# Optimization experiments

Measured on AMD Instinct MI355X. Metric: run time of the kernel, lower is better.

## Reference

```python
import jax, jax.numpy as jnp
import numpy as np

HIDDEN = 1024
NUM_HEADS = 16
HOP_NUM = 1023  # seq_len = hop_num + 1 = 1024
ATT_SIZE = HIDDEN // NUM_HEADS
SCALE = ATT_SIZE ** (-0.5)
B, S = 8, HOP_NUM + 1


def setup_inputs() -> dict:
    key = jax.random.key(0)
    ks = jax.random.split(key, 13)
    lim = 1.0 / np.sqrt(HIDDEN)
    return {
        "q": jax.random.normal(ks[0], (B, S, HIDDEN), jnp.float32),
        "k": jax.random.normal(ks[1], (B, S, HIDDEN), jnp.float32),
        "v": jax.random.normal(ks[2], (B, S, HIDDEN), jnp.float32),
        "attn_bias": jax.random.normal(ks[3], (B, 1, S, S), jnp.float32),
        "Wq": jax.random.uniform(ks[4], (HIDDEN, HIDDEN), jnp.float32, -lim, lim),
        "bq": jax.random.uniform(ks[5], (HIDDEN,), jnp.float32, -lim, lim),
        "Wk": jax.random.uniform(ks[6], (HIDDEN, HIDDEN), jnp.float32, -lim, lim),
        "bk": jax.random.uniform(ks[7], (HIDDEN,), jnp.float32, -lim, lim),
        "Wv": jax.random.uniform(ks[8], (HIDDEN, HIDDEN), jnp.float32, -lim, lim),
        "bv": jax.random.uniform(ks[9], (HIDDEN,), jnp.float32, -lim, lim),
        "Wo": jax.random.uniform(ks[10], (HIDDEN, HIDDEN), jnp.float32, -lim, lim),
        "bo": jax.random.uniform(ks[11], (HIDDEN,), jnp.float32, -lim, lim),
        "zoom_bias": jax.random.normal(ks[12], (2 * HOP_NUM + 1, 1), jnp.float32),
    }


def reference(q, k, v, attn_bias, Wq, bq, Wk, bk, Wv, bv, Wo, bo, zoom_bias):
    b, s, _ = q.shape
    # projections -> [b, s, h, d]
    qh = (q @ Wq.T + bq).reshape(b, s, NUM_HEADS, ATT_SIZE)
    kh = (k @ Wk.T + bk).reshape(b, s, NUM_HEADS, ATT_SIZE)
    vh = (v @ Wv.T + bv).reshape(b, s, NUM_HEADS, ATT_SIZE)
    # relative zoom encoding: ze[i, j] = zoom_bias[i - j + hop_num]
    idx = jnp.arange(s)[:, None] - jnp.arange(s)[None, :] + HOP_NUM
    ze = zoom_bias[idx, 0]  # [s, s]
    # scaled dot-product attention with additive zoom bias
    scores = jnp.einsum("bshd,bthd->bhst", qh * SCALE, kh) + ze + attn_bias
    probs = jax.nn.softmax(scores, axis=-1)
    out = jnp.einsum("bhst,bthd->bshd", probs, vh).reshape(b, s, NUM_HEADS * ATT_SIZE)
    return out @ Wo.T + bo
```

## Files before the change

### kernel.cpp

```cpp
#include <hip/hip_runtime.h>
#include <cstdint>


#define SQ   1024
#define HID  1024
#define SCALE 0.125f

typedef __attribute__((ext_vector_type(8))) __bf16 bf16x8;
typedef __attribute__((ext_vector_type(8))) unsigned short ushort8;
typedef __attribute__((ext_vector_type(4))) float  floatx4;

__device__ __forceinline__ float b2f(unsigned short x) {
    return __builtin_bit_cast(float, (uint32_t)x << 16);
}
__device__ __forceinline__ unsigned short f2bf(float f) {
    uint32_t u = __builtin_bit_cast(uint32_t, f);
    u += 0x7fffu + ((u >> 16) & 1u);
    return (unsigned short)(u >> 16);
}

__device__ __forceinline__ void glds16(const void* g, void* l) {
    __builtin_amdgcn_global_load_lds(
        (const __attribute__((address_space(1))) void*)g,
        (__attribute__((address_space(3))) void*)l, 16, 0, 0);
}

__global__ void cvt(const float* __restrict__ s, unsigned short* __restrict__ d,
                    int n4, float scale) {
    const int i = blockIdx.x * blockDim.x + threadIdx.x;
    if (i >= n4) return;
    const floatx4 v = *(const floatx4*)(s + 4 * (size_t)i);
    uint32_t lo = (uint32_t)f2bf(v[0] * scale) | ((uint32_t)f2bf(v[1] * scale) << 16);
    uint32_t hi = (uint32_t)f2bf(v[2] * scale) | ((uint32_t)f2bf(v[3] * scale) << 16);
    ((uint2*)d)[i] = make_uint2(lo, hi);
}

template <bool TRANS>
__global__ __launch_bounds__(256) void gemm_bt(
    const short* __restrict__ A, const short* __restrict__ Bw,
    const float* __restrict__ bias, void* __restrict__ C, size_t cOff, int outF32)
{
    __shared__ __align__(16) short As[4096];
    __shared__ __align__(16) short Bs[4096];

    const int tid = threadIdx.x;
    const int w = tid >> 6, lane = tid & 63;
    const int quad = lane >> 4, c = lane & 15;
    const int wr = w >> 1, wc = w & 1;

    const int nwg = gridDim.x * gridDim.y;
    const int id  = blockIdx.y * gridDim.x + blockIdx.x;
    const int nid = (id & 7) * (nwg >> 3) + (id >> 3);
    const int bn = nid & 7, bm = nid >> 3;

    const short* ag0 = A  + (size_t)(bm * 128 + w * 16 + c) * HID + quad * 8;
    const short* ag1 = ag0 + (size_t)64 * HID;
    const short* bg0 = Bw + (size_t)(bn * 128 + w * 16 + c) * HID + quad * 8;
    const short* bg1 = bg0 + (size_t)64 * HID;

    floatx4 acc[4][4] = {};

    for (int kt = 0; kt < 32; ++kt) {
        __syncthreads();
        glds16(ag0, As + w * 512);
        glds16(ag1, As + (w + 4) * 512);
        glds16(bg0, Bs + w * 512);
        glds16(bg1, Bs + (w + 4) * 512);
        asm volatile("s_waitcnt vmcnt(0)" ::: "memory");
        __syncthreads();
        ag0 += 32; ag1 += 32; bg0 += 32; bg1 += 32;

        bf16x8 a[4], b[4];
#pragma unroll
        for (int i = 0; i < 4; ++i)
            a[i] = *(const bf16x8*)(As + (wr * 4 + i) * 512 + lane * 8);
#pragma unroll
        for (int j = 0; j < 4; ++j)
            b[j] = *(const bf16x8*)(Bs + (wc * 4 + j) * 512 + lane * 8);
#pragma unroll
        for (int i = 0; i < 4; ++i)
#pragma unroll
            for (int j = 0; j < 4; ++j)
                acc[i][j] = __builtin_amdgcn_mfma_f32_16x16x32_bf16(a[i], b[j], acc[i][j], 0, 0, 0);
    }

    float bsv[4];
#pragma unroll
    for (int j = 0; j < 4; ++j)
        bsv[j] = bias[bn * 128 + wc * 64 + j * 16 + c];

#pragma unroll
    for (int i = 0; i < 4; ++i) {
#pragma unroll
        for (int j = 0; j < 4; ++j) {
            const int n = bn * 128 + wc * 64 + j * 16 + c;
#pragma unroll
            for (int r = 0; r < 4; ++r) {
                const int row = bm * 128 + wr * 64 + i * 16 + quad * 4 + r;
                const float val = acc[i][j][r] + bsv[j];
                size_t idx;
                if (TRANS) idx = ((size_t)(row >> 10) * HID + n) * SQ + (row & 1023);
                else       idx = (size_t)row * HID + n;
                if (outF32) ((float*)C)[cOff + idx] = val;
                else        ((unsigned short*)C)[cOff + idx] = f2bf(val);
            }
        }
    }
}

__global__ __launch_bounds__(256) void attn(
    const short* __restrict__ qh, const short* __restrict__ kh,
    const short* __restrict__ vht, const unsigned short* __restrict__ abc,
    const float* __restrict__ zbf, short* __restrict__ aout, int b0)
{
    __shared__ __align__(16) short Kf[4096];
    __shared__ __align__(16) short Vf[4096];
    __shared__ __align__(16) short Ps[4][2304];
    __shared__ float Zs[1152];

    const int tid = threadIdx.x;
    const int w = tid >> 6, lane = tid & 63;
    const int quad = lane >> 4, c = lane & 15;
    const int qb = blockIdx.x, h = blockIdx.y, bl = blockIdx.z;
    const int b = b0 + bl;

    for (int j = tid; j < 1151; j += 256)
        Zs[j] = zbf[qb * 128 + j];

    const size_t blS = (size_t)bl * SQ;

    bf16x8 qa[2][2];
#pragma unroll
    for (int m = 0; m < 2; ++m)
#pragma unroll
        for (int half = 0; half < 2; ++half)
            qa[m][half] = *(const bf16x8*)(qh + (blS + qb * 128 + w * 32 + m * 16 + c) * HID
                                               + h * 64 + half * 32 + quad * 8);

    const short* kg = kh  + (blS + 2 * c + (w & 1)) * HID + h * 64 + (w >> 1) * 32 + quad * 8;
    const short* vg = vht + ((size_t)bl * HID + h * 64 + w * 16 + c) * SQ + quad * 8;
    const size_t bge = ((size_t)b * SQ + qb * 128 + w * 32 + quad * 4) * SQ;

    bf16x8 kv0 = *(const bf16x8*)kg, kv1 = *(const bf16x8*)(kg + 32 * HID);
    bf16x8 vv0 = *(const bf16x8*)vg, vv1 = *(const bf16x8*)(vg + 32);

    floatx4 o[2][4] = {};
    float sume[2][4] = {};

    for (int kt = 0; kt < 16; ++kt) {
        __syncthreads();
        *(bf16x8*)(Kf + w * 512 + lane * 8)       = kv0;
        *(bf16x8*)(Kf + (w + 4) * 512 + lane * 8) = kv1;
        *(bf16x8*)(Vf + w * 512 + lane * 8)       = vv0;
        *(bf16x8*)(Vf + (w + 4) * 512 + lane * 8) = vv1;
        __syncthreads();

        if (kt < 15) {
            kg += 64 * HID; vg += 64;
            kv0 = *(const bf16x8*)kg; kv1 = *(const bf16x8*)(kg + 32 * HID);
            vv0 = *(const bf16x8*)vg; vv1 = *(const bf16x8*)(vg + 32);
        }

        floatx4 sc[2][2][2] = {};
#pragma unroll
        for (int sub = 0; sub < 2; ++sub) {
            bf16x8 kf[2][2];
#pragma unroll
            for (int half = 0; half < 2; ++half)
#pragma unroll
                for (int kb = 0; kb < 2; ++kb)
                    kf[half][kb] = *(const bf16x8*)(Kf + (sub * 4 + half * 2 + kb) * 512 + lane * 8);
#pragma unroll
            for (int m = 0; m < 2; ++m)
#pragma unroll
                for (int kb = 0; kb < 2; ++kb) {
                    sc[m][sub][kb] = __builtin_amdgcn_mfma_f32_16x16x32_bf16(qa[m][0], kf[0][kb], sc[m][sub][kb], 0, 0, 0);
                    sc[m][sub][kb] = __builtin_amdgcn_mfma_f32_16x16x32_bf16(qa[m][1], kf[1][kb], sc[m][sub][kb], 0, 0, 0);
                }
        }

        const int k0 = kt * 64;
#pragma unroll
        for (int m = 0; m < 2; ++m) {
#pragma unroll
            for (int r = 0; r < 4; ++r) {
                const int lrq = w * 32 + m * 16 + quad * 4 + r;
                const int tb = lrq + 1023 - k0;
                const size_t brow = bge + (size_t)(m * 16 + r) * SQ + k0;
#pragma unroll
                for (int sub = 0; sub < 2; ++sub) {
                    const int kl = sub * 32 + 2 * c;
                    const uint32_t bp = *(const uint32_t*)(abc + brow + kl);
                    const float z0 = Zs[tb - kl], z1 = Zs[tb - kl - 1];
                    const float s0 = sc[m][sub][0][r] * SCALE + z0 + b2f((unsigned short)(bp & 0xffffu));
                    const float s1 = sc[m][sub][1][r] * SCALE + z1
                                   + __builtin_bit_cast(float, bp & 0xffff0000u);
                    const float e0 = __expf(s0), e1 = __expf(s1);
                    sume[m][r] += e0 + e1;
                    const uint32_t pp = (uint32_t)f2bf(e0) | ((uint32_t)f2bf(e1) << 16);
                    *(uint32_t*)(&Ps[w][0] + (m * 16 + quad * 4 + r) * 72 + kl) = pp;
                }
            }
        }

#pragma unroll
        for (int sub = 0; sub < 2; ++sub) {
            bf16x8 ap[2];
#pragma unroll
            for (int m = 0; m < 2; ++m)
                ap[m] = *(const bf16x8*)(&Ps[w][0] + (m * 16 + c) * 72 + sub * 32 + quad * 8);
#pragma unroll
            for (int dt = 0; dt < 4; ++dt) {
                const bf16x8 vf = *(const bf16x8*)(Vf + (sub * 4 + dt) * 512 + lane * 8);
#pragma unroll
                for (int m = 0; m < 2; ++m)
                    o[m][dt] = __builtin_amdgcn_mfma_f32_16x16x32_bf16(ap[m], vf, o[m][dt], 0, 0, 0);
            }
        }
    }

#pragma unroll
    for (int m = 0; m < 2; ++m)
#pragma unroll
        for (int r = 0; r < 4; ++r) {
            float s = sume[m][r];
            s += __shfl_xor(s, 1);
            s += __shfl_xor(s, 2);
            s += __shfl_xor(s, 4);
            s += __shfl_xor(s, 8);
            sume[m][r] = 1.0f / s;
        }

#pragma unroll
    for (int m = 0; m < 2; ++m)
#pragma unroll
        for (int dt = 0; dt < 4; ++dt)
#pragma unroll
            for (int r = 0; r < 4; ++r) {
                const size_t row = blS + qb * 128 + w * 32 + m * 16 + quad * 4 + r;
                ((unsigned short*)aout)[row * HID + h * 64 + dt * 16 + c] =
                    f2bf(o[m][dt][r] * sume[m][r]);
            }
}

extern "C" void kernel_launch(void* const* d_in, const int* in_sizes, int n_in,
                              void* d_out, int out_size, void* d_ws, size_t ws_size,
                              hipStream_t stream) {
    const float* q  = (const float*)d_in[0];
    const float* k  = (const float*)d_in[1];
    const float* v  = (const float*)d_in[2];
    const float* ab = (const float*)d_in[3];
    const float* Wq = (const float*)d_in[4];  const float* bq = (const float*)d_in[5];
    const float* Wk = (const float*)d_in[6];  const float* bk = (const float*)d_in[7];
    const float* Wv = (const float*)d_in[8];  const float* bv = (const float*)d_in[9];
    const float* Wo = (const float*)d_in[10]; const float* bo = (const float*)d_in[11];
    const float* zb = (const float*)d_in[12];

    const size_t perB = (size_t)SQ * HID;
    const size_t WN   = (size_t)HID * HID;

    int G = 8;
    while (G > 1 && 24ull * 1024 * 1024 + 8ull * G * perB > ws_size) G >>= 1;

    unsigned short* Wqc = (unsigned short*)d_ws;
    unsigned short* Wkc = Wqc + WN;
    unsigned short* Wvc = Wkc + WN;
    unsigned short* Woc = Wvc + WN;
    unsigned short* abc = Woc + WN;
    short* cb  = (short*)(abc + 8 * perB);
    short* qh  = cb  + (size_t)G * perB;
    short* khp = qh  + (size_t)G * perB;
    short* vht = khp + (size_t)G * perB;
    short* ao  = cb;

    const dim3 bt(256);
    const dim3 gg(8, G * 8);
    const int ngroups = 8 / G;
    const int cn4 = (int)(G * perB / 4);
    const int cgrid = (cn4 + 255) / 256;

    cvt<<<(WN / 4 + 255) / 256, 256, 0, stream>>>(Wq, Wqc, WN / 4, 1.0f);
    cvt<<<(WN / 4 + 255) / 256, 256, 0, stream>>>(Wk, Wkc, WN / 4, 1.0f);
    cvt<<<(WN / 4 + 255) / 256, 256, 0, stream>>>(Wv, Wvc, WN / 4, 1.0f);
    cvt<<<(WN / 4 + 255) / 256, 256, 0, stream>>>(Wo, Woc, WN / 4, 1.0f);
    cvt<<<(8 * perB / 4 + 255) / 256, 256, 0, stream>>>(ab, abc, 8 * perB / 4, 1.0f);

    for (int g = 0; g < ngroups; ++g) {
        const size_t off = (size_t)g * G * perB;
        cvt<<<cgrid, 256, 0, stream>>>(q + off, (unsigned short*)cb, cn4, 1.0f);
        gemm_bt<false><<<gg, bt, 0, stream>>>(cb, (short*)Wqc, bq, qh, 0, 0);
        cvt<<<cgrid, 256, 0, stream>>>(k + off, (unsigned short*)cb, cn4, 1.0f);
        gemm_bt<false><<<gg, bt, 0, stream>>>(cb, (short*)Wkc, bk, khp, 0, 0);
        cvt<<<cgrid, 256, 0, stream>>>(v + off, (unsigned short*)cb, cn4, 1.0f);
        gemm_bt<true ><<<gg, bt, 0, stream>>>(cb, (short*)Wvc, bv, vht, 0, 0);
        attn<<<dim3(8, 16, G), bt, 0, stream>>>(qh, khp, vht, abc, zb, ao, g * G);
        gemm_bt<false><<<gg, bt, 0, stream>>>(ao, (short*)Woc, bo, d_out, off, 1);
    }
}
```

Before: 518.1 us.

## Batch QKV conversion and projection launches, prefetch bias, use exp2 softmax

Merges the three per-projection conversion kernels and the three projection GEMMs into single launches indexed by blockIdx.z, and gives the output GEMM its own f32-only kernel. In attention, the attn_bias tile for the next key block is prefetched into registers one iteration early. The softmax folds log2(e) into the score scale, zoom bias and pre-converted attn_bias so it can use exp2 directly. Extra workspace is needed for three separate converted input buffers, which may shrink the group size on small workspaces, and the register prefetch raises register pressure.

```diff
diff --git a/kernel.cpp b/kernel.cpp
--- a/kernel.cpp
+++ b/kernel.cpp
@@ -4,7 +4,8 @@
 
 #define SQ   1024
 #define HID  1024
-#define SCALE 0.125f
+#define CEXP 0.18033688f
+#define LOG2E 1.44269504f
 
 typedef __attribute__((ext_vector_type(8))) __bf16 bf16x8;
 typedef __attribute__((ext_vector_type(8))) unsigned short ushort8;
@@ -35,13 +36,38 @@
     ((uint2*)d)[i] = make_uint2(lo, hi);
 }
 
-template <bool TRANS>
-__global__ __launch_bounds__(256) void gemm_bt(
-    const short* __restrict__ A, const short* __restrict__ Bw,
-    const float* __restrict__ bias, void* __restrict__ C, size_t cOff, int outF32)
+__global__ void cvt3(const float* __restrict__ s0, const float* __restrict__ s1,
+                     const float* __restrict__ s2, unsigned short* __restrict__ d0,
+                     unsigned short* __restrict__ d1, unsigned short* __restrict__ d2,
+                     int n4) {
+    const int i = blockIdx.x * blockDim.x + threadIdx.x;
+    if (i >= n4) return;
+    const int z = blockIdx.y;
+    const float* s = z == 0 ? s0 : (z == 1 ? s1 : s2);
+    unsigned short* d = z == 0 ? d0 : (z == 1 ? d1 : d2);
+    const floatx4 v = *(const floatx4*)(s + 4 * (size_t)i);
+    uint32_t lo = (uint32_t)f2bf(v[0]) | ((uint32_t)f2bf(v[1]) << 16);
+    uint32_t hi = (uint32_t)f2bf(v[2]) | ((uint32_t)f2bf(v[3]) << 16);
+    ((uint2*)d)[i] = make_uint2(lo, hi);
+}
+
+__global__ __launch_bounds__(256) void gemm_qkv(
+    const short* __restrict__ Aq, const short* __restrict__ Ak,
+    const short* __restrict__ Av, const short* __restrict__ Wq_,
+    const short* __restrict__ Wk_, const short* __restrict__ Wv_,
+    const float* __restrict__ bq_, const float* __restrict__ bk_,
+    const float* __restrict__ bv_, short* __restrict__ oq,
+    short* __restrict__ ok, short* __restrict__ ov)
 {
     __shared__ __align__(16) short As[4096];
     __shared__ __align__(16) short Bs[4096];
+
+    const int z = blockIdx.z;
+    const short* A    = z == 0 ? Aq  : (z == 1 ? Ak  : Av);
+    const short* Bw   = z == 0 ? Wq_ : (z == 1 ? Wk_ : Wv_);
+    const float* bias = z == 0 ? bq_ : (z == 1 ? bk_ : bv_);
+    short* C          = z == 0 ? oq  : (z == 1 ? ok  : ov);
+    const bool trans  = (z == 2);
 
     const int tid = threadIdx.x;
     const int w = tid >> 6, lane = tid & 63;
@@ -98,14 +124,79 @@
             for (int r = 0; r < 4; ++r) {
                 const int row = bm * 128 + wr * 64 + i * 16 + quad * 4 + r;
                 const float val = acc[i][j][r] + bsv[j];
-                size_t idx;
-                if (TRANS) idx = ((size_t)(row >> 10) * HID + n) * SQ + (row & 1023);
-                else       idx = (size_t)row * HID + n;
-                if (outF32) ((float*)C)[cOff + idx] = val;
-                else        ((unsigned short*)C)[cOff + idx] = f2bf(val);
+                const size_t idx = trans
+                    ? ((size_t)(row >> 10) * HID + n) * SQ + (row & 1023)
+                    : (size_t)row * HID + n;
+                C[idx] = (short)f2bf(val);
             }
         }
     }
+}
+
+__global__ __launch_bounds__(256) void gemm_bt(
+    const short* __restrict__ A, const short* __restrict__ Bw,
+    const float* __restrict__ bias, float* __restrict__ C, size_t cOff)
+{
+    __shared__ __align__(16) short As[4096];
+    __shared__ __align__(16) short Bs[4096];
+
+    const int tid = threadIdx.x;
+    const int w = tid >> 6, lane = tid & 63;
+    const int quad = lane >> 4, c = lane & 15;
+    const int wr = w >> 1, wc = w & 1;
+
+    const int nwg = gridDim.x * gridDim.y;
+    const int id  = blockIdx.y * gridDim.x + blockIdx.x;
+    const int nid = (id & 7) * (nwg >> 3) + (id >> 3);
+    const int bn = nid & 7, bm = nid >> 3;
+
+    const short* ag0 = A  + (size_t)(bm * 128 + w * 16 + c) * HID + quad * 8;
+    const short* ag1 = ag0 + (size_t)64 * HID;
+    const short* bg0 = Bw + (size_t)(bn * 128 + w * 16 + c) * HID + quad * 8;
+    const short* bg1 = bg0 + (size_t)64 * HID;
+
+    floatx4 acc[4][4] = {};
+
+    for (int kt = 0; kt < 32; ++kt) {
+        __syncthreads();
+        glds16(ag0, As + w * 512);
+        glds16(ag1, As + (w + 4) * 512);
+        glds16(bg0, Bs + w * 512);
+        glds16(bg1, Bs + (w + 4) * 512);
+        asm volatile("s_waitcnt vmcnt(0)" ::: "memory");
+        __syncthreads();
+        ag0 += 32; ag1 += 32; bg0 += 32; bg1 += 32;
+
+        bf16x8 a[4], b[4];
+#pragma unroll
+        for (int i = 0; i < 4; ++i)
+            a[i] = *(const bf16x8*)(As + (wr * 4 + i) * 512 + lane * 8);
+#pragma unroll
+        for (int j = 0; j < 4; ++j)
+            b[j] = *(const bf16x8*)(Bs + (wc * 4 + j) * 512 + lane * 8);
+#pragma unroll
+        for (int i = 0; i < 4; ++i)
+#pragma unroll
+            for (int j = 0; j < 4; ++j)
+                acc[i][j] = __builtin_amdgcn_mfma_f32_16x16x32_bf16(a[i], b[j], acc[i][j], 0, 0, 0);
+    }
+
+    float bsv[4];
+#pragma unroll
+    for (int j = 0; j < 4; ++j)
+        bsv[j] = bias[bn * 128 + wc * 64 + j * 16 + c];
+
+#pragma unroll
+    for (int i = 0; i < 4; ++i)
+#pragma unroll
+        for (int j = 0; j < 4; ++j) {
+            const int n = bn * 128 + wc * 64 + j * 16 + c;
+#pragma unroll
+            for (int r = 0; r < 4; ++r) {
+                const int row = bm * 128 + wr * 64 + i * 16 + quad * 4 + r;
+                C[cOff + (size_t)row * HID + n] = acc[i][j][r] + bsv[j];
+            }
+        }
 }
 
 __global__ __launch_bounds__(256) void attn(
@@ -125,7 +216,7 @@
     const int b = b0 + bl;
 
     for (int j = tid; j < 1151; j += 256)
-        Zs[j] = zbf[qb * 128 + j];
+        Zs[j] = zbf[qb * 128 + j] * LOG2E;
 
     const size_t blS = (size_t)bl * SQ;
 
@@ -143,6 +234,19 @@
 
     bf16x8 kv0 = *(const bf16x8*)kg, kv1 = *(const bf16x8*)(kg + 32 * HID);
     bf16x8 vv0 = *(const bf16x8*)vg, vv1 = *(const bf16x8*)(vg + 32);
+
+    uint32_t bp[2][4][2];
+    auto loadB = [&](int K0) {
+#pragma unroll
+        for (int m = 0; m < 2; ++m)
+#pragma unroll
+            for (int r = 0; r < 4; ++r)
+#pragma unroll
+                for (int sub = 0; sub < 2; ++sub)
+                    bp[m][r][sub] = *(const uint32_t*)(abc + bge + (size_t)(m * 16 + r) * SQ
+                                                        + K0 + sub * 32 + 2 * c);
+    };
+    loadB(0);
 
     floatx4 o[2][4] = {};
     float sume[2][4] = {};
@@ -186,22 +290,24 @@
             for (int r = 0; r < 4; ++r) {
                 const int lrq = w * 32 + m * 16 + quad * 4 + r;
                 const int tb = lrq + 1023 - k0;
-                const size_t brow = bge + (size_t)(m * 16 + r) * SQ + k0;
 #pragma unroll
                 for (int sub = 0; sub < 2; ++sub) {
                     const int kl = sub * 32 + 2 * c;
-                    const uint32_t bp = *(const uint32_t*)(abc + brow + kl);
+                    const uint32_t bv_ = bp[m][r][sub];
                     const float z0 = Zs[tb - kl], z1 = Zs[tb - kl - 1];
-                    const float s0 = sc[m][sub][0][r] * SCALE + z0 + b2f((unsigned short)(bp & 0xffffu));
-                    const float s1 = sc[m][sub][1][r] * SCALE + z1
-                                   + __builtin_bit_cast(float, bp & 0xffff0000u);
-                    const float e0 = __expf(s0), e1 = __expf(s1);
+                    const float s0 = sc[m][sub][0][r] * CEXP + z0 + b2f((unsigned short)(bv_ & 0xffffu));
+                    const float s1 = sc[m][sub][1][r] * CEXP + z1
+                                   + __builtin_bit_cast(float, bv_ & 0xffff0000u);
+                    const float e0 = __builtin_amdgcn_exp2f(s0);
+                    const float e1 = __builtin_amdgcn_exp2f(s1);
                     sume[m][r] += e0 + e1;
                     const uint32_t pp = (uint32_t)f2bf(e0) | ((uint32_t)f2bf(e1) << 16);
                     *(uint32_t*)(&Ps[w][0] + (m * 16 + quad * 4 + r) * 72 + kl) = pp;
                 }
             }
         }
+
+        if (kt < 15) loadB(k0 + 64);
 
 #pragma unroll
         for (int sub = 0; sub < 2; ++sub) {
@@ -260,21 +366,22 @@
     const size_t WN   = (size_t)HID * HID;
 
     int G = 8;
-    while (G > 1 && 24ull * 1024 * 1024 + 8ull * G * perB > ws_size) G >>= 1;
+    while (G > 1 && 24ull * 1024 * 1024 + 12ull * G * perB > ws_size) G >>= 1;
 
     unsigned short* Wqc = (unsigned short*)d_ws;
     unsigned short* Wkc = Wqc + WN;
     unsigned short* Wvc = Wkc + WN;
     unsigned short* Woc = Wvc + WN;
     unsigned short* abc = Woc + WN;
-    short* cb  = (short*)(abc + 8 * perB);
-    short* qh  = cb  + (size_t)G * perB;
+    short* cbq = (short*)(abc + 8 * perB);
+    short* cbk = cbq + (size_t)G * perB;
+    short* cbv = cbk + (size_t)G * perB;
+    short* qh  = cbv + (size_t)G * perB;
     short* khp = qh  + (size_t)G * perB;
     short* vht = khp + (size_t)G * perB;
-    short* ao  = cb;
+    short* ao  = cbq;
 
     const dim3 bt(256);
-    const dim3 gg(8, G * 8);
     const int ngroups = 8 / G;
     const int cn4 = (int)(G * perB / 4);
     const int cgrid = (cn4 + 255) / 256;
@@ -283,17 +390,17 @@
     cvt<<<(WN / 4 + 255) / 256, 256, 0, stream>>>(Wk, Wkc, WN / 4, 1.0f);
     cvt<<<(WN / 4 + 255) / 256, 256, 0, stream>>>(Wv, Wvc, WN / 4, 1.0f);
     cvt<<<(WN / 4 + 255) / 256, 256, 0, stream>>>(Wo, Woc, WN / 4, 1.0f);
-    cvt<<<(8 * perB / 4 + 255) / 256, 256, 0, stream>>>(ab, abc, 8 * perB / 4, 1.0f);
+    cvt<<<(8 * perB / 4 + 255) / 256, 256, 0, stream>>>(ab, abc, 8 * perB / 4, LOG2E);
 
     for (int g = 0; g < ngroups; ++g) {
         const size_t off = (size_t)g * G * perB;
-        cvt<<<cgrid, 256, 0, stream>>>(q + off, (unsigned short*)cb, cn4, 1.0f);
-        gemm_bt<false><<<gg, bt, 0, stream>>>(cb, (short*)Wqc, bq, qh, 0, 0);
-        cvt<<<cgrid, 256, 0, stream>>>(k + off, (unsigned short*)cb, cn4, 1.0f);
-        gemm_bt<false><<<gg, bt, 0, stream>>>(cb, (short*)Wkc, bk, khp, 0, 0);
-        cvt<<<cgrid, 256, 0, stream>>>(v + off, (unsigned short*)cb, cn4, 1.0f);
-        gemm_bt<true ><<<gg, bt, 0, stream>>>(cb, (short*)Wvc, bv, vht, 0, 0);
+        cvt3<<<dim3(cgrid, 3), 256, 0, stream>>>(
+            q + off, k + off, v + off,
+            (unsigned short*)cbq, (unsigned short*)cbk, (unsigned short*)cbv, cn4);
+        gemm_qkv<<<dim3(8, G * 8, 3), bt, 0, stream>>>(
+            cbq, cbk, cbv, (short*)Wqc, (short*)Wkc, (short*)Wvc,
+            bq, bk, bv, qh, khp, vht);
         attn<<<dim3(8, 16, G), bt, 0, stream>>>(qh, khp, vht, abc, zb, ao, g * G);
-        gemm_bt<false><<<gg, bt, 0, stream>>>(ao, (short*)Woc, bo, d_out, off, 1);
+        gemm_bt<<<dim3(8, G * 8), bt, 0, stream>>>(ao, (short*)Woc, bo, (float*)d_out, off);
     }
 }
```

After: 421.0 us. -18.7%, faster.
